# Kernel tuning notes

Hardware: AMD Instinct MI355X
Metric: run time of the kernel (lower is better)

Reference implementation:

```python
import jax, jax.numpy as jnp
import numpy as np

N = 50000
E = 400000
F_IN = 5
H = 8
C1, C2, C3 = 64, 32, 16
NEG_SLOPE = 0.2


def setup_inputs() -> dict:
    key = jax.random.key(0)
    ks = jax.random.split(key, 16)
    s = 0.1  # small init scale
    return {
        "x": jax.random.normal(ks[0], (N, F_IN), jnp.float32),
        "edge_index": jax.random.randint(ks[1], (2, E), 0, N, jnp.int64),
        "edge_weight": jax.random.uniform(ks[2], (E,), jnp.float32),
        "W1": jax.random.normal(ks[3], (F_IN, H * C1), jnp.float32) * s,
        "a_src1": jax.random.normal(ks[4], (H, C1), jnp.float32) * s,
        "a_dst1": jax.random.normal(ks[5], (H, C1), jnp.float32) * s,
        "b1": jnp.zeros((H * C1,), jnp.float32),
        "W2": jax.random.normal(ks[6], (H * C1, H * C2), jnp.float32) * s,
        "a_src2": jax.random.normal(ks[7], (H, C2), jnp.float32) * s,
        "a_dst2": jax.random.normal(ks[8], (H, C2), jnp.float32) * s,
        "b2": jnp.zeros((H * C2,), jnp.float32),
        "Wg": jax.random.normal(ks[9], (H * C2, C3), jnp.float32) * s,
        "bg": jnp.zeros((C3,), jnp.float32),
        "Wfc": jax.random.normal(ks[10], (C3, 1), jnp.float32) * s,
        "bfc": jnp.zeros((1,), jnp.float32),
    }


def _gat_layer(x, W, a_src, a_dst, b, src, dst, n, heads, ch):
    # PyG GATConv (concat=True), eval mode (dropout off), self-loops already in src/dst.
    h = (x @ W).reshape(n, heads, ch)                      # (N, H, C)
    e_s = jnp.sum(h * a_src, axis=-1)                      # (N, H)
    e_d = jnp.sum(h * a_dst, axis=-1)                      # (N, H)
    e = jax.nn.leaky_relu(e_s[src] + e_d[dst], NEG_SLOPE)  # (Etot, H)
    m = jax.ops.segment_max(e, dst, num_segments=n)
    m = jnp.where(jnp.isfinite(m), m, 0.0)                 # guard empty segments
    ex = jnp.exp(e - m[dst])
    den = jax.ops.segment_sum(ex, dst, num_segments=n)
    alpha = ex / (den[dst] + 1e-16)                        # softmax over in-edges
    out = jax.ops.segment_sum(h[src] * alpha[..., None], dst, num_segments=n)
    return out.reshape(n, heads * ch) + b


def _gcn_layer(x, W, b, src, dst, w_full, n):
    # PyG GCNConv with gcn_norm: D^{-1/2} A_hat D^{-1/2}, self-loop weight 1.
    deg = jax.ops.segment_sum(w_full, dst, num_segments=n)
    dinv = jnp.where(deg > 0, jax.lax.rsqrt(deg), 0.0)
    norm = dinv[src] * w_full * dinv[dst]                  # (Etot,)
    h = x @ W                                              # (N, C3)
    out = jax.ops.segment_sum(h[src] * norm[:, None], dst, num_segments=n)
    return out + b


def reference(x, edge_index, edge_weight, W1, a_src1, a_dst1, b1,
              W2, a_src2, a_dst2, b2, Wg, bg, Wfc, bfc):
    n = x.shape[0]
    loops = jnp.arange(n, dtype=edge_index.dtype)
    src = jnp.concatenate([edge_index[0], loops])
    dst = jnp.concatenate([edge_index[1], loops])
    w_full = jnp.concatenate([edge_weight, jnp.ones((n,), edge_weight.dtype)])

    h = _gat_layer(x, W1, a_src1, a_dst1, b1, src, dst, n, H, C1)
    h = jax.nn.elu(h)
    h = _gat_layer(h, W2, a_src2, a_dst2, b2, src, dst, n, H, C2)
    h = jax.nn.elu(h)
    h = _gcn_layer(h, Wg, bg, src, dst, w_full, n)
    h = jax.nn.elu(h)
    out = jax.nn.sigmoid(h @ Wfc + bfc)                    # (N, 1)
    return out
```

## Files before the change

kernel.cpp:

```cpp
#include <hip/hip_runtime.h>
#include <hip/hip_bf16.h>
#include <float.h>
#include <math.h>

#define N_NODES 50000
#define N_EDGES 400000
#define ETOT    (N_EDGES + N_NODES)
#define F_IN    5
#define HEADS   8
#define C1      64
#define C2      32
#define C3      16
#define HC1     (HEADS * C1)
#define HC2     (HEADS * C2)
#define NEG_SLOPE 0.2f
#define NCHUNK  ((N_NODES + 255) / 256)
#define NH8     (N_NODES * HEADS)
#define MPAD    (((N_NODES + 63) / 64) * 64)
#define GCOLS   (HC2 + 16)
#define PACKBLK ((GCOLS * HC1) / 256)
#define SCATBLK ((ETOT + 255) / 256)
#define ES1BLK  ((NH8 + 255) / 256)
#define INIT_DEG  ((N_EDGES + 255) / 256)
#define INIT_W2X  (INIT_DEG + PACKBLK)
#define INIT_TOT  (INIT_W2X + ES1BLK)

#define WFIX_SCALE 68719476736.0f
#define WFIX_MASK  ((1ULL << 46) - 1)

typedef short bf16x8 __attribute__((ext_vector_type(8)));
typedef float f32x4  __attribute__((ext_vector_type(4)));
typedef unsigned short ushort_t;
typedef unsigned short ushort8_t __attribute__((ext_vector_type(8)));

__device__ __forceinline__ float eluf(float x) {
    return x > 0.f ? x : (expf(x) - 1.f);
}
__device__ __forceinline__ float bf2f(unsigned short u) {
    union { unsigned int i; float f; } v; v.i = ((unsigned int)u) << 16; return v.f;
}
__device__ __forceinline__ unsigned short f2bf(float f) {
    __hip_bfloat16 b = __float2bfloat16(f);
    return *(unsigned short*)&b;
}
__device__ __forceinline__ float softnum(float es, float ed) {
    float v = es + ed;
    v = v > 0.f ? v : NEG_SLOPE * v;
    return expf(v);
}

__global__ void k_init(const int* __restrict__ ei, const float* __restrict__ ew,
                       unsigned long long* __restrict__ pack,
                       ushort_t* __restrict__ rank,
                       const float* __restrict__ x, float* __restrict__ xp8,
                       const float* __restrict__ W2,
                       const float* __restrict__ a_src2, const float* __restrict__ a_dst2,
                       ushort_t* __restrict__ W2X,
                       const float* __restrict__ W1,
                       const float* __restrict__ a_src1, const float* __restrict__ a_dst1,
                       float* __restrict__ es, float* __restrict__ ed) {
    __shared__ float asl[HEADS * F_IN], adl[HEADS * F_IN];
    int b = blockIdx.x;
    int t = threadIdx.x;
    if (b < INIT_DEG) {
        int i = b * 256 + t;
        if (i >= N_EDGES) return;
        int d   = ei[N_EDGES + i];
        float w = ew[i];
        unsigned long long enc =
            (1ULL << 46) | (unsigned long long)(w * WFIX_SCALE + 0.5f);
        unsigned long long old = atomicAdd(&pack[d], enc);
        rank[i] = (ushort_t)(old >> 46);
    } else if (b < INIT_W2X) {
        int idx = (b - INIT_DEG) * 256 + t;
        int c = idx >> 9;
        int k = idx & 511;
        float v;
        if (c < HC2) {
            v = W2[(size_t)k * HC2 + c];
        } else {
            int h = (c - HC2) & 7;
            const float* av = (c < HC2 + 8) ? a_src2 : a_dst2;
            v = 0.f;
#pragma unroll 8
            for (int j = 0; j < C2; j++)
                v += W2[(size_t)k * HC2 + h * C2 + j] * av[h * C2 + j];
        }
        W2X[idx] = f2bf(v);
    } else {
        if (t < HEADS * F_IN) {
            int h = t / F_IN, f = t % F_IN;
            float s = 0.f, dv = 0.f;
            for (int c = 0; c < C1; c++) {
                float wv = W1[f * HC1 + h * C1 + c];
                s  += wv * a_src1[h * C1 + c];
                dv += wv * a_dst1[h * C1 + c];
            }
            asl[t] = s;
            adl[t] = dv;
        }
        __syncthreads();
        int g = (b - INIT_W2X) * 256 + t;
        if (g < NH8) {
            int n = g >> 3, h = g & 7;
            float vs = 0.f, vd = 0.f;
#pragma unroll
            for (int f = 0; f < F_IN; f++) {
                float xv = x[n * F_IN + f];
                vs += xv * asl[h * F_IN + f];
                vd += xv * adl[h * F_IN + f];
            }
            es[g] = vs;
            ed[g] = vd;
            xp8[g] = (h < F_IN) ? x[n * F_IN + h] : 0.f;
        }
    }
}

__global__ void k_scan_a(const unsigned long long* __restrict__ pack,
                         int* __restrict__ part) {
    __shared__ int lds[256];
    int t = threadIdx.x;
    int i = blockIdx.x * 256 + t;
    lds[t] = (i < N_NODES) ? (int)(pack[i] >> 46) + 1 : 0;
    __syncthreads();
    for (int off = 128; off >= 1; off >>= 1) {
        if (t < off) lds[t] += lds[t + off];
        __syncthreads();
    }
    if (t == 0) part[blockIdx.x] = lds[0];
}

__global__ void k_scan_b(int* part) {
    __shared__ int lds[256];
    int t = threadIdx.x;
    int v = (t < NCHUNK) ? part[t] : 0;
    lds[t] = v;
    __syncthreads();
    for (int off = 1; off < 256; off <<= 1) {
        int x = (t >= off) ? lds[t - off] : 0;
        __syncthreads();
        lds[t] += x;
        __syncthreads();
    }
    if (t < NCHUNK) part[t] = lds[t] - v;
}

__global__ void k_scan_c(const unsigned long long* __restrict__ pack,
                         const int* __restrict__ part,
                         int* __restrict__ offs, float* __restrict__ dinv) {
    __shared__ int lds[256];
    int t = threadIdx.x;
    int i = blockIdx.x * 256 + t;
    unsigned long long p = (i < N_NODES) ? pack[i] : 0ULL;
    int v = (i < N_NODES) ? (int)(p >> 46) + 1 : 0;
    lds[t] = v;
    __syncthreads();
    for (int off = 1; off < 256; off <<= 1) {
        int x = (t >= off) ? lds[t - off] : 0;
        __syncthreads();
        lds[t] += x;
        __syncthreads();
    }
    int excl = part[blockIdx.x] + lds[t] - v;
    if (i < N_NODES) {
        offs[i] = excl;
        float wsum = (float)(p & WFIX_MASK) * (1.0f / WFIX_SCALE) + 1.0f;
        dinv[i] = rsqrtf(wsum);
    }
    if (i == N_NODES - 1) offs[N_NODES] = excl + v;
}

__global__ void k_scatter(const int* __restrict__ ei, const int* __restrict__ offs,
                          const ushort_t* __restrict__ rank, int2* __restrict__ csr,
                          const float* __restrict__ ew, const float* __restrict__ dinv) {
    int i = blockIdx.x * 256 + threadIdx.x;
    if (i >= ETOT) return;
    int s, d, pos;
    float w;
    if (i < N_EDGES) {
        s = ei[i]; d = ei[N_EDGES + i]; w = ew[i];
        pos = offs[d] + (int)rank[i];
    } else {
        s = d = i - N_EDGES; w = 1.f;
        pos = offs[d + 1] - 1;
    }
    float nrm = dinv[s] * w * dinv[d];
    csr[pos] = make_int2(s, __float_as_int(nrm));
}

__global__ __launch_bounds__(256) void k_aggexp(const float* __restrict__ xp8,
                                                const float* __restrict__ es1,
                                                const float* __restrict__ ed1,
                                                const int* __restrict__ offs,
                                                const int2* __restrict__ csr,
                                                const float* __restrict__ W1,
                                                const float* __restrict__ b1,
                                                ushort_t* __restrict__ x2bf) {
    __shared__ float ax[256 * F_IN];
    int t = threadIdx.x;
    int g = blockIdx.x * 256 + t;
    if (g < NH8) {
        int d = g >> 3, h = g & 7;
        float edv = ed1[g];
        int k0 = offs[d], k1 = offs[d + 1];
        float a0 = 0.f, a1 = 0.f, a2 = 0.f, a3 = 0.f, a4 = 0.f, exsum = 0.f;
        int k = k0;
        for (; k + 3 < k1; k += 4) {
            int2 c0 = csr[k], c1 = csr[k + 1], c2 = csr[k + 2], c3 = csr[k + 3];
            float r0 = es1[c0.x * HEADS + h];
            float r1 = es1[c1.x * HEADS + h];
            float r2 = es1[c2.x * HEADS + h];
            float r3 = es1[c3.x * HEADS + h];
            float4 A0 = *(const float4*)(xp8 + (size_t)c0.x * 8);
            float  B0 = xp8[(size_t)c0.x * 8 + 4];
            float4 A1 = *(const float4*)(xp8 + (size_t)c1.x * 8);
            float  B1 = xp8[(size_t)c1.x * 8 + 4];
            float4 A2 = *(const float4*)(xp8 + (size_t)c2.x * 8);
            float  B2 = xp8[(size_t)c2.x * 8 + 4];
            float4 A3 = *(const float4*)(xp8 + (size_t)c3.x * 8);
            float  B3 = xp8[(size_t)c3.x * 8 + 4];
            float x0 = softnum(r0, edv);
            float x1 = softnum(r1, edv);
            float x2 = softnum(r2, edv);
            float x3 = softnum(r3, edv);
            a0 += x0 * A0.x + x1 * A1.x + x2 * A2.x + x3 * A3.x;
            a1 += x0 * A0.y + x1 * A1.y + x2 * A2.y + x3 * A3.y;
            a2 += x0 * A0.z + x1 * A1.z + x2 * A2.z + x3 * A3.z;
            a3 += x0 * A0.w + x1 * A1.w + x2 * A2.w + x3 * A3.w;
            a4 += x0 * B0   + x1 * B1   + x2 * B2   + x3 * B3;
            exsum += (x0 + x1) + (x2 + x3);
        }
        for (; k < k1; k++) {
            int2 c0 = csr[k];
            float x0 = softnum(es1[c0.x * HEADS + h], edv);
            float4 A0 = *(const float4*)(xp8 + (size_t)c0.x * 8);
            float  B0 = xp8[(size_t)c0.x * 8 + 4];
            a0 += x0 * A0.x;
            a1 += x0 * A0.y;
            a2 += x0 * A0.z;
            a3 += x0 * A0.w;
            a4 += x0 * B0;
            exsum += x0;
        }
        float inv = 1.f / (exsum + 1e-16f);
        float* ap = ax + t * F_IN;
        ap[0] = a0 * inv;
        ap[1] = a1 * inv;
        ap[2] = a2 * inv;
        ap[3] = a3 * inv;
        ap[4] = a4 * inv;
    }
    __syncthreads();
    int wave = t >> 6, j = t & 63;
    int n0 = blockIdx.x * 32;
    int h = j >> 3;
    const float* w1p = W1 + j * 8;
#pragma unroll 1
    for (int it = 0; it < 8; ++it) {
        int nl = wave * 8 + it;
        int n = n0 + nl;
        if (n >= N_NODES) break;
        const float* ap = ax + (nl * 8 + h) * F_IN;
        float av[F_IN];
#pragma unroll
        for (int f = 0; f < F_IN; f++) av[f] = ap[f];
        float4 s0 = *(const float4*)(b1 + j * 8);
        float4 s1 = *(const float4*)(b1 + j * 8 + 4);
#pragma unroll
        for (int f = 0; f < F_IN; f++) {
            float4 w0  = *(const float4*)(w1p + f * HC1);
            float4 w1v = *(const float4*)(w1p + f * HC1 + 4);
            s0.x += av[f] * w0.x;  s0.y += av[f] * w0.y;
            s0.z += av[f] * w0.z;  s0.w += av[f] * w0.w;
            s1.x += av[f] * w1v.x; s1.y += av[f] * w1v.y;
            s1.z += av[f] * w1v.z; s1.w += av[f] * w1v.w;
        }
        ushort8_t o;
        o[0] = f2bf(eluf(s0.x)); o[1] = f2bf(eluf(s0.y));
        o[2] = f2bf(eluf(s0.z)); o[3] = f2bf(eluf(s0.w));
        o[4] = f2bf(eluf(s1.x)); o[5] = f2bf(eluf(s1.y));
        o[6] = f2bf(eluf(s1.z)); o[7] = f2bf(eluf(s1.w));
        *(ushort8_t*)(x2bf + (size_t)n * HC1 + j * 8) = o;
    }
}

__global__ __launch_bounds__(256, 3) void k_gemm_mfma(const short* __restrict__ A,
                                                      const short* __restrict__ W2X,
                                                      ushort_t* __restrict__ h2bf,
                                                      float* __restrict__ es2,
                                                      float* __restrict__ ed2) {
    __shared__ short Bs[GCOLS * 32];
    int t    = threadIdx.x;
    int wave = t >> 6;
    int lane = t & 63;
    int lo   = lane & 15;
    int quad = lane >> 4;
    int m0   = blockIdx.x * 64 + wave * 16;
    const short* ap = A + (size_t)(m0 + lo) * HC1 + quad * 8;

    f32x4 acc[17];
#pragma unroll
    for (int f = 0; f < 17; f++) acc[f] = (f32x4){0.f, 0.f, 0.f, 0.f};

    for (int idx = t; idx < GCOLS * 4; idx += 256) {
        int c = idx >> 2, q = idx & 3;
        int s = (q + c + (c >> 2)) & 3;
        *(bf16x8*)(Bs + c * 32 + s * 8) = *(const bf16x8*)(W2X + (size_t)c * HC1 + q * 8);
    }
    __syncthreads();

#pragma unroll 1
    for (int k0 = 0; k0 < HC1; k0 += 32) {
        int nk = k0 + 32;
        bf16x8 pre[5];
        if (nk < HC1) {
#pragma unroll
            for (int j = 0; j < 5; j++) {
                int idx = t + j * 256;
                if (idx < GCOLS * 4) {
                    int c = idx >> 2, q = idx & 3;
                    pre[j] = *(const bf16x8*)(W2X + (size_t)c * HC1 + nk + q * 8);
                }
            }
        }
        bf16x8 aF = *(const bf16x8*)(ap + k0);
#pragma unroll
        for (int f = 0; f < 17; f++) {
            int c = f * 16 + lo;
            int s = (quad + c + (c >> 2)) & 3;
            bf16x8 bF = *(const bf16x8*)(Bs + c * 32 + s * 8);
            acc[f] = __builtin_amdgcn_mfma_f32_16x16x32_bf16(aF, bF, acc[f], 0, 0, 0);
        }
        __syncthreads();
        if (nk < HC1) {
#pragma unroll
            for (int j = 0; j < 5; j++) {
                int idx = t + j * 256;
                if (idx < GCOLS * 4) {
                    int c = idx >> 2, q = idx & 3;
                    int s = (q + c + (c >> 2)) & 3;
                    *(bf16x8*)(Bs + c * 32 + s * 8) = pre[j];
                }
            }
            __syncthreads();
        }
    }

    int rowb = m0 + quad * 4;
#pragma unroll
    for (int f = 0; f < 16; f++) {
#pragma unroll
        for (int r = 0; r < 4; r++) {
            int row = rowb + r;
            if (row < N_NODES)
                h2bf[(size_t)row * HC2 + f * 16 + lo] = f2bf(acc[f][r]);
        }
    }
#pragma unroll
    for (int r = 0; r < 4; r++) {
        int row = rowb + r;
        if (row < N_NODES) {
            if (lo < 8) es2[row * HEADS + lo]       = acc[16][r];
            else        ed2[row * HEADS + (lo - 8)] = acc[16][r];
        }
    }
}

__global__ __launch_bounds__(128) void k_gat_agg2(const ushort_t* __restrict__ h2bf,
                                                  const float* __restrict__ es2,
                                                  const float* __restrict__ ed2,
                                                  const int* __restrict__ offs,
                                                  const int2* __restrict__ csr,
                                                  const float* __restrict__ b2,
                                                  ushort_t* __restrict__ x3bf) {
    int wave = threadIdx.x >> 6;
    int lane = threadIdx.x & 63;
    int d = blockIdx.x * 2 + wave;
    if (d >= N_NODES) return;
    int c4 = lane * 4;
    int h  = lane >> 3;
    float edv = ed2[d * HEADS + h];
    int k0 = offs[d], k1 = offs[d + 1];
    float acc0 = 0.f, acc1 = 0.f, acc2 = 0.f, acc3 = 0.f, exsum = 0.f;
    int k = k0;
    for (; k + 3 < k1; k += 4) {
        int2 e0 = csr[k], e1 = csr[k + 1], e2 = csr[k + 2], e3 = csr[k + 3];
        float r0 = es2[e0.x * HEADS + h];
        float r1 = es2[e1.x * HEADS + h];
        float r2 = es2[e2.x * HEADS + h];
        float r3 = es2[e3.x * HEADS + h];
        ushort4 v0 = *(const ushort4*)(h2bf + (size_t)e0.x * HC2 + c4);
        ushort4 v1 = *(const ushort4*)(h2bf + (size_t)e1.x * HC2 + c4);
        ushort4 v2 = *(const ushort4*)(h2bf + (size_t)e2.x * HC2 + c4);
        ushort4 v3 = *(const ushort4*)(h2bf + (size_t)e3.x * HC2 + c4);
        float x0 = softnum(r0, edv);
        float x1 = softnum(r1, edv);
        float x2 = softnum(r2, edv);
        float x3 = softnum(r3, edv);
        acc0 += x0 * bf2f(v0.x) + x1 * bf2f(v1.x) + x2 * bf2f(v2.x) + x3 * bf2f(v3.x);
        acc1 += x0 * bf2f(v0.y) + x1 * bf2f(v1.y) + x2 * bf2f(v2.y) + x3 * bf2f(v3.y);
        acc2 += x0 * bf2f(v0.z) + x1 * bf2f(v1.z) + x2 * bf2f(v2.z) + x3 * bf2f(v3.z);
        acc3 += x0 * bf2f(v0.w) + x1 * bf2f(v1.w) + x2 * bf2f(v2.w) + x3 * bf2f(v3.w);
        exsum += (x0 + x1) + (x2 + x3);
    }
    for (; k < k1; k++) {
        int2 e0 = csr[k];
        float x0 = softnum(es2[e0.x * HEADS + h], edv);
        ushort4 v0 = *(const ushort4*)(h2bf + (size_t)e0.x * HC2 + c4);
        acc0 += x0 * bf2f(v0.x);
        acc1 += x0 * bf2f(v0.y);
        acc2 += x0 * bf2f(v0.z);
        acc3 += x0 * bf2f(v0.w);
        exsum += x0;
    }
    float inv = 1.f / (exsum + 1e-16f);
    float4 bias = *(const float4*)(b2 + c4);
    ushort4 o;
    o.x = f2bf(eluf(acc0 * inv + bias.x));
    o.y = f2bf(eluf(acc1 * inv + bias.y));
    o.z = f2bf(eluf(acc2 * inv + bias.z));
    o.w = f2bf(eluf(acc3 * inv + bias.w));
    *(ushort4*)(x3bf + (size_t)d * HC2 + c4) = o;
}

__global__ __launch_bounds__(256) void k_hg(const ushort_t* __restrict__ x3bf,
                                            const float* __restrict__ Wg,
                                            float* __restrict__ hg) {
    __shared__ float xs[16 * 260];
    int n0 = blockIdx.x * 16;
    int t  = threadIdx.x;
    for (int q = t; q < 16 * HC2 / 4; q += 256) {
        int r  = q >> 6;
        int cc = (q & 63) * 4;
        int n  = n0 + r;
        ushort4 v = make_ushort4(0, 0, 0, 0);
        if (n < N_NODES) v = *(const ushort4*)(x3bf + (size_t)n * HC2 + cc);
        xs[r * 260 + cc + 0] = bf2f(v.x);
        xs[r * 260 + cc + 1] = bf2f(v.y);
        xs[r * 260 + cc + 2] = bf2f(v.z);
        xs[r * 260 + cc + 3] = bf2f(v.w);
    }
    __syncthreads();
    int r = t >> 4, c = t & 15;
    const float* xr = xs + r * 260;
    float acc = 0.f;
#pragma unroll 8
    for (int k = 0; k < HC2; k += 4) {
        float4 v = *(const float4*)(xr + k);
        acc += v.x * Wg[(k + 0) * C3 + c];
        acc += v.y * Wg[(k + 1) * C3 + c];
        acc += v.z * Wg[(k + 2) * C3 + c];
        acc += v.w * Wg[(k + 3) * C3 + c];
    }
    int n = n0 + r;
    if (n < N_NODES) hg[(size_t)n * C3 + c] = acc;
}

__global__ __launch_bounds__(256) void k_gcn_out(const float* __restrict__ hg,
                                                 const int* __restrict__ offs,
                                                 const int2* __restrict__ csr,
                                                 const float* __restrict__ bg,
                                                 const float* __restrict__ Wfc,
                                                 const float* __restrict__ bfc,
                                                 float* __restrict__ out) {
    int t = threadIdx.x;
    int r = t >> 4, c = t & 15;
    int d = blockIdx.x * 16 + r;
    float val = 0.f;
    if (d < N_NODES) {
        int k0 = offs[d], k1 = offs[d + 1];
        float acc = 0.f;
        int k = k0;
        for (; k + 3 < k1; k += 4) {
            int2 e0 = csr[k], e1 = csr[k + 1], e2 = csr[k + 2], e3 = csr[k + 3];
            float g0 = hg[(size_t)e0.x * C3 + c];
            float g1 = hg[(size_t)e1.x * C3 + c];
            float g2 = hg[(size_t)e2.x * C3 + c];
            float g3 = hg[(size_t)e3.x * C3 + c];
            acc += g0 * __int_as_float(e0.y) + g1 * __int_as_float(e1.y)
                 + g2 * __int_as_float(e2.y) + g3 * __int_as_float(e3.y);
        }
        for (; k < k1; k++) {
            int2 e0 = csr[k];
            acc += hg[(size_t)e0.x * C3 + c] * __int_as_float(e0.y);
        }
        val = eluf(acc + bg[c]);
    }
    float z = val * Wfc[c];
#pragma unroll
    for (int off = 8; off >= 1; off >>= 1) z += __shfl_xor(z, off, 16);
    if (c == 0 && d < N_NODES) out[d] = 1.f / (1.f + expf(-(z + bfc[0])));
}

extern "C" void kernel_launch(void* const* d_in, const int* in_sizes, int n_in,
                              void* d_out, int out_size, void* d_ws, size_t ws_size,
                              hipStream_t stream) {
    const float* x       = (const float*)d_in[0];
    const int*   ei      = (const int*)  d_in[1];
    const float* ew      = (const float*)d_in[2];
    const float* W1      = (const float*)d_in[3];
    const float* a_src1  = (const float*)d_in[4];
    const float* a_dst1  = (const float*)d_in[5];
    const float* b1      = (const float*)d_in[6];
    const float* W2      = (const float*)d_in[7];
    const float* a_src2  = (const float*)d_in[8];
    const float* a_dst2  = (const float*)d_in[9];
    const float* b2      = (const float*)d_in[10];
    const float* Wg      = (const float*)d_in[11];
    const float* bg      = (const float*)d_in[12];
    const float* Wfc     = (const float*)d_in[13];
    const float* bfc     = (const float*)d_in[14];
    float* out = (float*)d_out;

    char* w = (char*)d_ws;
    size_t off = 0;
    auto alloc = [&](size_t bytes) -> void* {
        void* p = w + off;
        off = (off + bytes + 255) & ~(size_t)255;
        return p;
    };
    ushort_t* x2bf = (ushort_t*)alloc((size_t)MPAD * HC1 * 2);
    ushort_t* W2X  = (ushort_t*)alloc((size_t)GCOLS * HC1 * 2);
    ushort_t* h2bf = (ushort_t*)alloc((size_t)N_NODES * HC2 * 2);
    ushort_t* x3bf = (ushort_t*)alloc((size_t)N_NODES * HC2 * 2);
    float* hg     = (float*)alloc((size_t)N_NODES * C3 * 4);
    float* es1    = (float*)alloc((size_t)NH8 * 4);
    float* ed1    = (float*)alloc((size_t)NH8 * 4);
    float* es2    = (float*)alloc((size_t)NH8 * 4);
    float* ed2    = (float*)alloc((size_t)NH8 * 4);
    unsigned long long* pack = (unsigned long long*)alloc((size_t)N_NODES * 8);
    char*  zero_end = w + off;
    ushort_t* rank = (ushort_t*)alloc((size_t)N_EDGES * 2);
    int*   offs   = (int*)  alloc((size_t)(N_NODES + 1) * 4);
    int*   part   = (int*)  alloc(256 * 4);
    int2*  csr    = (int2*) alloc((size_t)ETOT * 8);
    float* dinv   = (float*)alloc((size_t)N_NODES * 4);
    float* xp8    = (float*)alloc((size_t)N_NODES * 8 * 4);

    hipMemsetAsync(pack, 0, (size_t)(zero_end - (char*)pack), stream);
    k_init<<<dim3(INIT_TOT), dim3(256), 0, stream>>>(
        ei, ew, pack, rank, x, xp8, W2, a_src2, a_dst2, W2X,
        W1, a_src1, a_dst1, es1, ed1);
    k_scan_a<<<dim3(NCHUNK), dim3(256), 0, stream>>>(pack, part);
    k_scan_b<<<dim3(1), dim3(256), 0, stream>>>(part);
    k_scan_c<<<dim3(NCHUNK), dim3(256), 0, stream>>>(pack, part, offs, dinv);
    k_scatter<<<dim3(SCATBLK), dim3(256), 0, stream>>>(ei, offs, rank, csr, ew, dinv);

    k_aggexp<<<dim3(ES1BLK), dim3(256), 0, stream>>>(
        xp8, es1, ed1, offs, csr, W1, b1, x2bf);

    k_gemm_mfma<<<dim3(MPAD / 64), dim3(256), 0, stream>>>(
        (const short*)x2bf, (const short*)W2X, h2bf, es2, ed2);
    k_gat_agg2<<<dim3((N_NODES + 1) / 2), dim3(128), 0, stream>>>(
        h2bf, es2, ed2, offs, csr, b2, x3bf);

    k_hg<<<dim3((N_NODES + 15) / 16), dim3(256), 0, stream>>>(x3bf, Wg, hg);
    k_gcn_out<<<dim3((N_NODES + 15) / 16), dim3(256), 0, stream>>>(
        hg, offs, csr, bg, Wfc, bfc, out);
}
```

Before: 276.9 us.

## Fuse GCN projection into GAT layer-2 aggregation via wave shuffle reduction

New measurement: 325.6 us. +17.6%, slower.

```diff
diff --git a/kernel.cpp b/kernel.cpp
--- a/kernel.cpp
+++ b/kernel.cpp
@@ -373,7 +373,8 @@
                                                   const int* __restrict__ offs,
                                                   const int2* __restrict__ csr,
                                                   const float* __restrict__ b2,
-                                                  ushort_t* __restrict__ x3bf) {
+                                                  const float* __restrict__ Wg,
+                                                  float* __restrict__ hg) {
     int wave = threadIdx.x >> 6;
     int lane = threadIdx.x & 63;
     int d = blockIdx.x * 2 + wave;
@@ -416,45 +417,73 @@
     }
     float inv = 1.f / (exsum + 1e-16f);
     float4 bias = *(const float4*)(b2 + c4);
-    ushort4 o;
-    o.x = f2bf(eluf(acc0 * inv + bias.x));
-    o.y = f2bf(eluf(acc1 * inv + bias.y));
-    o.z = f2bf(eluf(acc2 * inv + bias.z));
-    o.w = f2bf(eluf(acc3 * inv + bias.w));
-    *(ushort4*)(x3bf + (size_t)d * HC2 + c4) = o;
-}
-
-__global__ __launch_bounds__(256) void k_hg(const ushort_t* __restrict__ x3bf,
-                                            const float* __restrict__ Wg,
-                                            float* __restrict__ hg) {
-    __shared__ float xs[16 * 260];
-    int n0 = blockIdx.x * 16;
-    int t  = threadIdx.x;
-    for (int q = t; q < 16 * HC2 / 4; q += 256) {
-        int r  = q >> 6;
-        int cc = (q & 63) * 4;
-        int n  = n0 + r;
-        ushort4 v = make_ushort4(0, 0, 0, 0);
-        if (n < N_NODES) v = *(const ushort4*)(x3bf + (size_t)n * HC2 + cc);
-        xs[r * 260 + cc + 0] = bf2f(v.x);
-        xs[r * 260 + cc + 1] = bf2f(v.y);
-        xs[r * 260 + cc + 2] = bf2f(v.z);
-        xs[r * 260 + cc + 3] = bf2f(v.w);
-    }
-    __syncthreads();
-    int r = t >> 4, c = t & 15;
-    const float* xr = xs + r * 260;
-    float acc = 0.f;
-#pragma unroll 8
-    for (int k = 0; k < HC2; k += 4) {
-        float4 v = *(const float4*)(xr + k);
-        acc += v.x * Wg[(k + 0) * C3 + c];
-        acc += v.y * Wg[(k + 1) * C3 + c];
-        acc += v.z * Wg[(k + 2) * C3 + c];
-        acc += v.w * Wg[(k + 3) * C3 + c];
-    }
-    int n = n0 + r;
-    if (n < N_NODES) hg[(size_t)n * C3 + c] = acc;
+    float q0 = eluf(acc0 * inv + bias.x);
+    float q1 = eluf(acc1 * inv + bias.y);
+    float q2 = eluf(acc2 * inv + bias.z);
+    float q3 = eluf(acc3 * inv + bias.w);
+
+    float p[16];
+    {
+        const float4* w0 = (const float4*)(Wg + (c4 + 0) * C3);
+        const float4* w1 = (const float4*)(Wg + (c4 + 1) * C3);
+        const float4* w2 = (const float4*)(Wg + (c4 + 2) * C3);
+        const float4* w3 = (const float4*)(Wg + (c4 + 3) * C3);
+#pragma unroll
+        for (int cb = 0; cb < 4; cb++) {
+            float4 a = w0[cb], b = w1[cb], c = w2[cb], e = w3[cb];
+            p[cb * 4 + 0] = q0 * a.x + q1 * b.x + q2 * c.x + q3 * e.x;
+            p[cb * 4 + 1] = q0 * a.y + q1 * b.y + q2 * c.y + q3 * e.y;
+            p[cb * 4 + 2] = q0 * a.z + q1 * b.z + q2 * c.z + q3 * e.z;
+            p[cb * 4 + 3] = q0 * a.w + q1 * b.w + q2 * c.w + q3 * e.w;
+        }
+    }
+    {
+        float tt[16];
+#pragma unroll
+        for (int c = 0; c < 16; c++) tt[c] = __shfl_xor(p[c], 1, 64);
+        if ((lane & 1) == 0) {
+#pragma unroll
+            for (int c = 0; c < 8; c++) p[c] = p[c] + tt[c];
+        } else {
+#pragma unroll
+            for (int c = 0; c < 8; c++) p[c] = p[c + 8] + tt[c + 8];
+        }
+    }
+    {
+        float tt[8];
+#pragma unroll
+        for (int c = 0; c < 8; c++) tt[c] = __shfl_xor(p[c], 2, 64);
+        if ((lane & 2) == 0) {
+#pragma unroll
+            for (int c = 0; c < 4; c++) p[c] = p[c] + tt[c];
+        } else {
+#pragma unroll
+            for (int c = 0; c < 4; c++) p[c] = p[c + 4] + tt[c + 4];
+        }
+    }
+    {
+        float tt[4];
+#pragma unroll
+        for (int c = 0; c < 4; c++) tt[c] = __shfl_xor(p[c], 4, 64);
+        if ((lane & 4) == 0) {
+            p[0] = p[0] + tt[0];
+            p[1] = p[1] + tt[1];
+        } else {
+            p[0] = p[2] + tt[2];
+            p[1] = p[3] + tt[3];
+        }
+    }
+    {
+        float t0 = __shfl_xor(p[0], 8, 64);
+        float t1 = __shfl_xor(p[1], 8, 64);
+        p[0] = ((lane & 8) == 0) ? (p[0] + t0) : (p[1] + t1);
+    }
+    p[0] += __shfl_xor(p[0], 16, 64);
+    p[0] += __shfl_xor(p[0], 32, 64);
+    if (lane < 16) {
+        int cw = ((lane & 1) << 3) | ((lane & 2) << 1) | ((lane & 4) >> 1) | ((lane & 8) >> 3);
+        hg[(size_t)d * C3 + cw] = p[0];
+    }
 }
 
 __global__ __launch_bounds__(256) void k_gcn_out(const float* __restrict__ hg,
@@ -523,7 +552,6 @@
     ushort_t* x2bf = (ushort_t*)alloc((size_t)MPAD * HC1 * 2);
     ushort_t* W2X  = (ushort_t*)alloc((size_t)GCOLS * HC1 * 2);
     ushort_t* h2bf = (ushort_t*)alloc((size_t)N_NODES * HC2 * 2);
-    ushort_t* x3bf = (ushort_t*)alloc((size_t)N_NODES * HC2 * 2);
     float* hg     = (float*)alloc((size_t)N_NODES * C3 * 4);
     float* es1    = (float*)alloc((size_t)NH8 * 4);
     float* ed1    = (float*)alloc((size_t)NH8 * 4);
@@ -553,9 +581,8 @@
     k_gemm_mfma<<<dim3(MPAD / 64), dim3(256), 0, stream>>>(
         (const short*)x2bf, (const short*)W2X, h2bf, es2, ed2);
     k_gat_agg2<<<dim3((N_NODES + 1) / 2), dim3(128), 0, stream>>>(
-        h2bf, es2, ed2, offs, csr, b2, x3bf);
-
-    k_hg<<<dim3((N_NODES + 15) / 16), dim3(256), 0, stream>>>(x3bf, Wg, hg);
+        h2bf, es2, ed2, offs, csr, b2, Wg, hg);
+
     k_gcn_out<<<dim3((N_NODES + 15) / 16), dim3(256), 0, stream>>>(
         hg, offs, csr, bg, Wfc, bfc, out);
 }
```
